# Kernel optimization log

Hardware: AMD Instinct MI355X
Metric: run time of the kernel (lower is better)

Reference implementation:

```python
import jax, jax.numpy as jnp
import numpy as np

S1 = 4096  # seq_len1
S2 = 4096  # seq_len2
D = 64     # in_dim1 == in_dim2
H = 2      # num_heads
KD = 1     # k_dim
VD = 1     # v_dim
EPS_NORM = 1e-12  # F.normalize eps
EPS_BN = 1e-5


def setup_inputs() -> dict:
    key = jax.random.key(0)
    ks = jax.random.split(key, 11)
    f = lambda k, s: jax.random.normal(k, s, dtype=jnp.float32)
    return {
        "x1": f(ks[0], (1, S1, D)),
        "x2": f(ks[1], (1, S2, D)),
        "Wq": f(ks[2], (D, H * KD)) * 0.1,   # proj_q1 (no bias)
        "Wk": f(ks[3], (D, H * KD)) * 0.1,   # proj_k2 (no bias)
        "Wv": f(ks[4], (D, H * VD)) * 0.1,   # proj_v2 (no bias)
        "Wo": f(ks[5], (H * VD, 2)) * 0.1,   # proj_o weight
        "bo": f(ks[6], (2,)) * 0.1,          # proj_o bias
        "Wg1": f(ks[7], (D, D)) * 0.1,       # CBN gamma MLP
        "Wg2": f(ks[8], (D, D)) * 0.1,
        "Wb1": f(ks[9], (D, D)) * 0.1,       # CBN beta MLP
        "Wb2": f(ks[10], (D, D)) * 0.1,
    }


def _l2norm_rows(x):
    # F.normalize(x, p=2, dim=1): divide by max(||row||, eps)
    n = jnp.sqrt(jnp.sum(x * x, axis=1, keepdims=True))
    return x / jnp.maximum(n, EPS_NORM)


def reference(x1, x2, Wq, Wk, Wv, Wo, bo, Wg1, Wg2, Wb1, Wb2):
    x1s, x2s = x1[0], x2[0]            # [S1,D], [S2,D] (batch squeezed, batch==1)
    # --- CBN stand-in: batchnorm of x2 conditioned on pooled x1 embedding ---
    h = x1s.mean(axis=0)               # [D]
    dg = jax.nn.relu(h @ Wg1) @ Wg2    # delta_gamma [D]
    db = jax.nn.relu(h @ Wb1) @ Wb2    # delta_beta  [D]
    mu = x2s.mean(axis=0)
    var = x2s.var(axis=0)
    v2_0 = (1.0 + dg) * (x2s - mu) * jax.lax.rsqrt(var + EPS_BN) + db  # [S2,D]
    # --- L2 normalizations ---
    v2n = _l2norm_rows(v2_0)[None]     # [1,S2,D]
    y1 = _l2norm_rows(x1s)[None]       # [1,S1,D]
    y2 = _l2norm_rows(x2s)[None]       # [1,S2,D]
    # --- tiny-head cross attention ---
    q = (y1 @ Wq).reshape(1, S1, H, KD)
    k = (y2 @ Wk).reshape(1, S2, H, KD)
    v = (v2n @ Wv).reshape(1, S2, H, VD)
    attn = jnp.einsum('bshk,bthk->bhst', q, k) / (KD ** 0.5)  # [1,H,S1,S2]
    attn = jax.nn.softmax(attn, axis=-1)
    out = jnp.einsum('bhst,bthd->bshd', attn, v).reshape(1, S1, H * VD)
    return jax.nn.sigmoid(out @ Wo + bo)  # [1,S1,2]
```

## Files before the change

### kernel.cpp

```cpp
#include <hip/hip_runtime.h>
#include <math.h>

#define NS1 4096
#define NS2 4096
#define ND  64

static constexpr int OFF_SUMX1 = 0;
static constexpr int OFF_SUMX2 = 64;
static constexpr int OFF_SSQX2 = 128;
static constexpr int OFF_SCALE = 192;
static constexpr int OFF_BETA  = 256;
static constexpr int OFF_MU    = 320;
static constexpr int OFF_KB    = 384;
static constexpr int OFF_Q     = 512;
static constexpr int OFF_KV    = 512 + 2 * 4096;
static constexpr int OFF_NUM   = OFF_KV + 4 * 4096;
static constexpr int OFF_DEN   = OFF_NUM + 2 * 4096;

__device__ inline float wred64(float v) {
    #pragma unroll
    for (int off = 32; off; off >>= 1) v += __shfl_xor(v, off);
    return v;
}

__global__ __launch_bounds__(256) void k_colred(const float* __restrict__ x1,
                                                const float* __restrict__ x2,
                                                float* __restrict__ ws) {
    int b = blockIdx.x;
    int tid = threadIdx.x;
    int w = tid >> 6, d = tid & 63;
    bool isx2 = (b >= 128);
    const float* x = isx2 ? x2 : x1;
    int row0 = (isx2 ? (b - 128) : b) * 32 + w * 8;
    float s = 0.f, ss = 0.f;
    #pragma unroll
    for (int i = 0; i < 8; ++i) {
        float v = x[(row0 + i) * ND + d];
        s += v; ss += v * v;
    }
    __shared__ float redS[256];
    __shared__ float redQ[256];
    redS[tid] = s; redQ[tid] = ss;
    __syncthreads();
    if (tid < 64) {
        float st = redS[tid] + redS[tid + 64] + redS[tid + 128] + redS[tid + 192];
        if (!isx2) {
            atomicAdd(&ws[OFF_SUMX1 + tid], st);
        } else {
            float sq = redQ[tid] + redQ[tid + 64] + redQ[tid + 128] + redQ[tid + 192];
            atomicAdd(&ws[OFF_SUMX2 + tid], st);
            atomicAdd(&ws[OFF_SSQX2 + tid], sq);
        }
    }
}

__global__ __launch_bounds__(64) void k_prep(const float* __restrict__ Wg1,
                                             const float* __restrict__ Wg2,
                                             const float* __restrict__ Wb1,
                                             const float* __restrict__ Wb2,
                                             const float* __restrict__ Wk,
                                             float* __restrict__ ws) {
    int d = threadIdx.x;
    __shared__ float h[64], ag[64], ab[64];
    h[d] = ws[OFF_SUMX1 + d] * (1.f / (float)NS1);
    __syncthreads();
    float tg = 0.f, tb = 0.f;
    #pragma unroll 8
    for (int j = 0; j < 64; ++j) {
        float hj = h[j];
        tg = fmaf(hj, Wg1[j * 64 + d], tg);
        tb = fmaf(hj, Wb1[j * 64 + d], tb);
    }
    ag[d] = fmaxf(tg, 0.f);
    ab[d] = fmaxf(tb, 0.f);
    __syncthreads();
    float dg = 0.f, db = 0.f;
    #pragma unroll 8
    for (int j = 0; j < 64; ++j) {
        dg = fmaf(ag[j], Wg2[j * 64 + d], dg);
        db = fmaf(ab[j], Wb2[j * 64 + d], db);
    }
    float mu = ws[OFF_SUMX2 + d] * (1.f / (float)NS2);
    float var = ws[OFF_SSQX2 + d] * (1.f / (float)NS2) - mu * mu;
    ws[OFF_SCALE + d] = (1.f + dg) * rsqrtf(var + 1e-5f);
    ws[OFF_BETA + d]  = db;
    ws[OFF_MU + d]    = mu;
    float k0 = Wk[d * 2 + 0], k1 = Wk[d * 2 + 1];
    float s0 = wred64(k0 * k0);
    float s1 = wred64(k1 * k1);
    if (d == 0) { ws[OFF_KB + 0] = sqrtf(s0); ws[OFF_KB + 1] = sqrtf(s1); }
}

__global__ __launch_bounds__(256) void k_proj(const float* __restrict__ x1,
                                              const float* __restrict__ x2,
                                              const float* __restrict__ Wq,
                                              const float* __restrict__ Wk,
                                              const float* __restrict__ Wv,
                                              float* __restrict__ ws) {
    int b = blockIdx.x;
    int w = threadIdx.x >> 6, d = threadIdx.x & 63;
    bool isx1 = (b >= 1024);
    int row = (isx1 ? (b - 1024) : b) * 4 + w;
    if (!isx1) {
        float x = x2[row * ND + d];
        float n2 = wred64(x * x);
        float y = x * (1.f / fmaxf(sqrtf(n2), 1e-12f));
        float vv = fmaf(ws[OFF_SCALE + d], x - ws[OFF_MU + d], ws[OFF_BETA + d]);
        float nv = wred64(vv * vv);
        float vn = vv * (1.f / fmaxf(sqrtf(nv), 1e-12f));
        float k0 = wred64(y  * Wk[d * 2 + 0]);
        float k1 = wred64(y  * Wk[d * 2 + 1]);
        float v0 = wred64(vn * Wv[d * 2 + 0]);
        float v1 = wred64(vn * Wv[d * 2 + 1]);
        if (d == 0) {
            ((float4*)(ws + OFF_KV))[row] = make_float4(k0, k1, v0, v1);
        }
    } else {
        float x = x1[row * ND + d];
        float n2 = wred64(x * x);
        float y = x * (1.f / fmaxf(sqrtf(n2), 1e-12f));
        float q0 = wred64(y * Wq[d * 2 + 0]);
        float q1 = wred64(y * Wq[d * 2 + 1]);
        if (d == 0) {
            ws[OFF_Q + row] = q0;
            ws[OFF_Q + NS1 + row] = q1;
        }
    }
}

__global__ __launch_bounds__(256) void k_attn(const float* __restrict__ wsc,
                                              float* __restrict__ ws) {
    __shared__ float4 kv[128];
    int b = blockIdx.x;
    int sc = b & 15, tc = b >> 4;
    int tid = threadIdx.x;
    const float4* kvg = (const float4*)(wsc + OFF_KV);
    if (tid < 128) kv[tid] = kvg[tc * 128 + tid];
    __syncthreads();
    int s = sc * 256 + tid;
    float q0 = wsc[OFF_Q + s];
    float q1 = wsc[OFF_Q + NS1 + s];
    float m0 = fabsf(q0) * wsc[OFF_KB + 0];
    float m1 = fabsf(q1) * wsc[OFF_KB + 1];
    float n0 = 0.f, d0 = 0.f, n1 = 0.f, d1 = 0.f;
    #pragma unroll 4
    for (int i = 0; i < 128; ++i) {
        float4 t = kv[i];
        float e0 = __expf(fmaf(q0, t.x, -m0));
        float e1 = __expf(fmaf(q1, t.y, -m1));
        n0 = fmaf(e0, t.z, n0); d0 += e0;
        n1 = fmaf(e1, t.w, n1); d1 += e1;
    }
    atomicAdd(&ws[OFF_NUM + s],        n0);
    atomicAdd(&ws[OFF_NUM + NS1 + s],  n1);
    atomicAdd(&ws[OFF_DEN + s],        d0);
    atomicAdd(&ws[OFF_DEN + NS1 + s],  d1);
}

__global__ __launch_bounds__(256) void k_out(const float* __restrict__ ws,
                                             const float* __restrict__ Wo,
                                             const float* __restrict__ bo,
                                             float* __restrict__ out) {
    int s = blockIdx.x * 256 + threadIdx.x;
    float o0 = ws[OFF_NUM + s]       / ws[OFF_DEN + s];
    float o1 = ws[OFF_NUM + NS1 + s] / ws[OFF_DEN + NS1 + s];
    float z0 = fmaf(o0, Wo[0], fmaf(o1, Wo[2], bo[0]));
    float z1 = fmaf(o0, Wo[1], fmaf(o1, Wo[3], bo[1]));
    out[s * 2 + 0] = 1.f / (1.f + __expf(-z0));
    out[s * 2 + 1] = 1.f / (1.f + __expf(-z1));
}

extern "C" void kernel_launch(void* const* d_in, const int* in_sizes, int n_in,
                              void* d_out, int out_size, void* d_ws, size_t ws_size,
                              hipStream_t stream) {
    const float* x1  = (const float*)d_in[0];
    const float* x2  = (const float*)d_in[1];
    const float* Wq  = (const float*)d_in[2];
    const float* Wk  = (const float*)d_in[3];
    const float* Wv  = (const float*)d_in[4];
    const float* Wo  = (const float*)d_in[5];
    const float* bo  = (const float*)d_in[6];
    const float* Wg1 = (const float*)d_in[7];
    const float* Wg2 = (const float*)d_in[8];
    const float* Wb1 = (const float*)d_in[9];
    const float* Wb2 = (const float*)d_in[10];
    float* ws  = (float*)d_ws;
    float* out = (float*)d_out;

    hipMemsetAsync((char*)d_ws + OFF_SUMX1 * 4, 0, 512 * 4, stream);
    hipMemsetAsync((char*)d_ws + OFF_NUM * 4,   0, 4 * NS1 * 4, stream);

    k_colred<<<256, 256, 0, stream>>>(x1, x2, ws);
    k_prep<<<1, 64, 0, stream>>>(Wg1, Wg2, Wb1, Wb2, Wk, ws);
    k_proj<<<2048, 256, 0, stream>>>(x1, x2, Wq, Wk, Wv, ws);
    k_attn<<<512, 256, 0, stream>>>(ws, ws);
    k_out<<<16, 256, 0, stream>>>(ws, Wo, bo, out);
}
```

Before: 100.2 us.

## Fuse prep into projection and attention into output, dropping atomics and a memset

Every projection block now recomputes the tiny CBN MLP redundantly instead of running a separate single-block prep kernel. Attention is restructured so each block owns 8 query rows over all 4096 keys, reducing in-block via shuffles and shared memory. This removes the global atomics, the NUM/DEN memset and the separate output kernel. It also switches to exp2f with pre-scaled log2e and cuts the launch count from five to three. The trade-off is redundant MLP work per block and higher register pressure from 8 rows of accumulators.

```diff
diff --git a/kernel.cpp b/kernel.cpp
--- a/kernel.cpp
+++ b/kernel.cpp
@@ -1,21 +1,14 @@
 #include <hip/hip_runtime.h>
 #include <math.h>
 
-#define NS1 4096
-#define NS2 4096
-#define ND  64
+#define NS 4096
+#define LOG2E 1.44269504088896f
 
 static constexpr int OFF_SUMX1 = 0;
 static constexpr int OFF_SUMX2 = 64;
 static constexpr int OFF_SSQX2 = 128;
-static constexpr int OFF_SCALE = 192;
-static constexpr int OFF_BETA  = 256;
-static constexpr int OFF_MU    = 320;
-static constexpr int OFF_KB    = 384;
-static constexpr int OFF_Q     = 512;
-static constexpr int OFF_KV    = 512 + 2 * 4096;
-static constexpr int OFF_NUM   = OFF_KV + 4 * 4096;
-static constexpr int OFF_DEN   = OFF_NUM + 2 * 4096;
+static constexpr int OFF_Q     = 256;
+static constexpr int OFF_KV    = 256 + 2*4096;
 
 __device__ inline float wred64(float v) {
     #pragma unroll
@@ -35,7 +28,7 @@
     float s = 0.f, ss = 0.f;
     #pragma unroll
     for (int i = 0; i < 8; ++i) {
-        float v = x[(row0 + i) * ND + d];
+        float v = x[(row0 + i) * 64 + d];
         s += v; ss += v * v;
     }
     __shared__ float redS[256];
@@ -54,120 +47,155 @@
     }
 }
 
-__global__ __launch_bounds__(64) void k_prep(const float* __restrict__ Wg1,
-                                             const float* __restrict__ Wg2,
-                                             const float* __restrict__ Wb1,
-                                             const float* __restrict__ Wb2,
-                                             const float* __restrict__ Wk,
-                                             float* __restrict__ ws) {
-    int d = threadIdx.x;
-    __shared__ float h[64], ag[64], ab[64];
-    h[d] = ws[OFF_SUMX1 + d] * (1.f / (float)NS1);
-    __syncthreads();
-    float tg = 0.f, tb = 0.f;
-    #pragma unroll 8
-    for (int j = 0; j < 64; ++j) {
-        float hj = h[j];
-        tg = fmaf(hj, Wg1[j * 64 + d], tg);
-        tb = fmaf(hj, Wb1[j * 64 + d], tb);
-    }
-    ag[d] = fmaxf(tg, 0.f);
-    ab[d] = fmaxf(tb, 0.f);
-    __syncthreads();
-    float dg = 0.f, db = 0.f;
-    #pragma unroll 8
-    for (int j = 0; j < 64; ++j) {
-        dg = fmaf(ag[j], Wg2[j * 64 + d], dg);
-        db = fmaf(ab[j], Wb2[j * 64 + d], db);
-    }
-    float mu = ws[OFF_SUMX2 + d] * (1.f / (float)NS2);
-    float var = ws[OFF_SSQX2 + d] * (1.f / (float)NS2) - mu * mu;
-    ws[OFF_SCALE + d] = (1.f + dg) * rsqrtf(var + 1e-5f);
-    ws[OFF_BETA + d]  = db;
-    ws[OFF_MU + d]    = mu;
-    float k0 = Wk[d * 2 + 0], k1 = Wk[d * 2 + 1];
-    float s0 = wred64(k0 * k0);
-    float s1 = wred64(k1 * k1);
-    if (d == 0) { ws[OFF_KB + 0] = sqrtf(s0); ws[OFF_KB + 1] = sqrtf(s1); }
-}
-
-__global__ __launch_bounds__(256) void k_proj(const float* __restrict__ x1,
-                                              const float* __restrict__ x2,
-                                              const float* __restrict__ Wq,
-                                              const float* __restrict__ Wk,
-                                              const float* __restrict__ Wv,
-                                              float* __restrict__ ws) {
-    int b = blockIdx.x;
-    int w = threadIdx.x >> 6, d = threadIdx.x & 63;
-    bool isx1 = (b >= 1024);
-    int row = (isx1 ? (b - 1024) : b) * 4 + w;
-    if (!isx1) {
-        float x = x2[row * ND + d];
-        float n2 = wred64(x * x);
-        float y = x * (1.f / fmaxf(sqrtf(n2), 1e-12f));
-        float vv = fmaf(ws[OFF_SCALE + d], x - ws[OFF_MU + d], ws[OFF_BETA + d]);
-        float nv = wred64(vv * vv);
-        float vn = vv * (1.f / fmaxf(sqrtf(nv), 1e-12f));
-        float k0 = wred64(y  * Wk[d * 2 + 0]);
-        float k1 = wred64(y  * Wk[d * 2 + 1]);
-        float v0 = wred64(vn * Wv[d * 2 + 0]);
-        float v1 = wred64(vn * Wv[d * 2 + 1]);
-        if (d == 0) {
-            ((float4*)(ws + OFF_KV))[row] = make_float4(k0, k1, v0, v1);
+__global__ __launch_bounds__(256) void k_prep_proj(const float* __restrict__ x1,
+                                                   const float* __restrict__ x2,
+                                                   const float* __restrict__ Wq,
+                                                   const float* __restrict__ Wk,
+                                                   const float* __restrict__ Wv,
+                                                   const float* __restrict__ Wg1,
+                                                   const float* __restrict__ Wg2,
+                                                   const float* __restrict__ Wb1,
+                                                   const float* __restrict__ Wb2,
+                                                   float* __restrict__ ws) {
+    int b = blockIdx.x, tid = threadIdx.x;
+    int w = tid >> 6, d = tid & 63;
+    if (b < 256) {
+        __shared__ float hsh[64], pg_[4][64], pb_[4][64], ag[64], ab[64];
+        __shared__ float scl[64], bta[64], mu[64];
+        if (tid < 64) hsh[tid] = ws[OFF_SUMX1 + tid] * (1.f / 4096.f);
+        __syncthreads();
+        float pg = 0.f, pb = 0.f;
+        #pragma unroll
+        for (int jj = 0; jj < 16; ++jj) {
+            int j = w * 16 + jj; float hj = hsh[j];
+            pg = fmaf(hj, Wg1[j * 64 + d], pg);
+            pb = fmaf(hj, Wb1[j * 64 + d], pb);
+        }
+        pg_[w][d] = pg; pb_[w][d] = pb;
+        __syncthreads();
+        if (w == 0) {
+            ag[d] = fmaxf(pg_[0][d] + pg_[1][d] + pg_[2][d] + pg_[3][d], 0.f);
+            ab[d] = fmaxf(pb_[0][d] + pb_[1][d] + pb_[2][d] + pb_[3][d], 0.f);
+        }
+        __syncthreads();
+        pg = 0.f; pb = 0.f;
+        #pragma unroll
+        for (int jj = 0; jj < 16; ++jj) {
+            int j = w * 16 + jj;
+            pg = fmaf(ag[j], Wg2[j * 64 + d], pg);
+            pb = fmaf(ab[j], Wb2[j * 64 + d], pb);
+        }
+        pg_[w][d] = pg; pb_[w][d] = pb;
+        __syncthreads();
+        if (w == 0) {
+            float dg = pg_[0][d] + pg_[1][d] + pg_[2][d] + pg_[3][d];
+            float db = pb_[0][d] + pb_[1][d] + pb_[2][d] + pb_[3][d];
+            float muv = ws[OFF_SUMX2 + d] * (1.f / 4096.f);
+            float var = ws[OFF_SSQX2 + d] * (1.f / 4096.f) - muv * muv;
+            scl[d] = (1.f + dg) * rsqrtf(var + 1e-5f);
+            bta[d] = db; mu[d] = muv;
+        }
+        __syncthreads();
+        float wk0 = Wk[d * 2 + 0], wk1 = Wk[d * 2 + 1];
+        float wv0 = Wv[d * 2 + 0], wv1 = Wv[d * 2 + 1];
+        float4* kvo = (float4*)(ws + OFF_KV);
+        #pragma unroll
+        for (int r = 0; r < 4; ++r) {
+            int row = b * 16 + w * 4 + r;
+            float x = x2[row * 64 + d];
+            float n2 = wred64(x * x);
+            float y = x * (1.f / fmaxf(sqrtf(n2), 1e-12f));
+            float vv = fmaf(scl[d], x - mu[d], bta[d]);
+            float nv = wred64(vv * vv);
+            float vn = vv * (1.f / fmaxf(sqrtf(nv), 1e-12f));
+            float k0 = wred64(y * wk0),  k1 = wred64(y * wk1);
+            float v0 = wred64(vn * wv0), v1 = wred64(vn * wv1);
+            if (d == 0) kvo[row] = make_float4(k0, k1, v0, v1);
         }
     } else {
-        float x = x1[row * ND + d];
-        float n2 = wred64(x * x);
-        float y = x * (1.f / fmaxf(sqrtf(n2), 1e-12f));
-        float q0 = wred64(y * Wq[d * 2 + 0]);
-        float q1 = wred64(y * Wq[d * 2 + 1]);
-        if (d == 0) {
-            ws[OFF_Q + row] = q0;
-            ws[OFF_Q + NS1 + row] = q1;
-        }
-    }
-}
-
-__global__ __launch_bounds__(256) void k_attn(const float* __restrict__ wsc,
-                                              float* __restrict__ ws) {
-    __shared__ float4 kv[128];
-    int b = blockIdx.x;
-    int sc = b & 15, tc = b >> 4;
-    int tid = threadIdx.x;
-    const float4* kvg = (const float4*)(wsc + OFF_KV);
-    if (tid < 128) kv[tid] = kvg[tc * 128 + tid];
-    __syncthreads();
-    int s = sc * 256 + tid;
-    float q0 = wsc[OFF_Q + s];
-    float q1 = wsc[OFF_Q + NS1 + s];
-    float m0 = fabsf(q0) * wsc[OFF_KB + 0];
-    float m1 = fabsf(q1) * wsc[OFF_KB + 1];
-    float n0 = 0.f, d0 = 0.f, n1 = 0.f, d1 = 0.f;
-    #pragma unroll 4
-    for (int i = 0; i < 128; ++i) {
-        float4 t = kv[i];
-        float e0 = __expf(fmaf(q0, t.x, -m0));
-        float e1 = __expf(fmaf(q1, t.y, -m1));
-        n0 = fmaf(e0, t.z, n0); d0 += e0;
-        n1 = fmaf(e1, t.w, n1); d1 += e1;
-    }
-    atomicAdd(&ws[OFF_NUM + s],        n0);
-    atomicAdd(&ws[OFF_NUM + NS1 + s],  n1);
-    atomicAdd(&ws[OFF_DEN + s],        d0);
-    atomicAdd(&ws[OFF_DEN + NS1 + s],  d1);
-}
-
-__global__ __launch_bounds__(256) void k_out(const float* __restrict__ ws,
-                                             const float* __restrict__ Wo,
-                                             const float* __restrict__ bo,
-                                             float* __restrict__ out) {
-    int s = blockIdx.x * 256 + threadIdx.x;
-    float o0 = ws[OFF_NUM + s]       / ws[OFF_DEN + s];
-    float o1 = ws[OFF_NUM + NS1 + s] / ws[OFF_DEN + NS1 + s];
-    float z0 = fmaf(o0, Wo[0], fmaf(o1, Wo[2], bo[0]));
-    float z1 = fmaf(o0, Wo[1], fmaf(o1, Wo[3], bo[1]));
-    out[s * 2 + 0] = 1.f / (1.f + __expf(-z0));
-    out[s * 2 + 1] = 1.f / (1.f + __expf(-z1));
+        float wq0 = Wq[d * 2 + 0], wq1 = Wq[d * 2 + 1];
+        #pragma unroll
+        for (int r = 0; r < 4; ++r) {
+            int row = (b - 256) * 16 + w * 4 + r;
+            float x = x1[row * 64 + d];
+            float n2 = wred64(x * x);
+            float y = x * (1.f / fmaxf(sqrtf(n2), 1e-12f));
+            float q0 = wred64(y * wq0), q1 = wred64(y * wq1);
+            if (d == 0) { ws[OFF_Q + row] = q0; ws[OFF_Q + 4096 + row] = q1; }
+        }
+    }
+}
+
+__global__ __launch_bounds__(256) void k_attn_out(const float* __restrict__ ws,
+                                                  const float* __restrict__ Wk,
+                                                  const float* __restrict__ Wo,
+                                                  const float* __restrict__ bo,
+                                                  float* __restrict__ out) {
+    int b = blockIdx.x, tid = threadIdx.x;
+    int w = tid >> 6, lane = tid & 63;
+    __shared__ float kb[2];
+    __shared__ float qsh[2][8];
+    if (w == 0) {
+        float c0 = Wk[lane * 2 + 0], c1 = Wk[lane * 2 + 1];
+        float s0 = wred64(c0 * c0), s1 = wred64(c1 * c1);
+        if (lane == 0) { kb[0] = sqrtf(s0); kb[1] = sqrtf(s1); }
+    }
+    if (tid >= 64 && tid < 72) {
+        int si = tid - 64;
+        qsh[0][si] = ws[OFF_Q + b * 8 + si];
+        qsh[1][si] = ws[OFF_Q + 4096 + b * 8 + si];
+    }
+    __syncthreads();
+    float q0r[8], q1r[8], m0r[8], m1r[8];
+    #pragma unroll
+    for (int si = 0; si < 8; ++si) {
+        q0r[si] = qsh[0][si] * LOG2E;
+        q1r[si] = qsh[1][si] * LOG2E;
+        m0r[si] = fabsf(q0r[si]) * kb[0];
+        m1r[si] = fabsf(q1r[si]) * kb[1];
+    }
+    float n0[8], d0[8], n1[8], d1[8];
+    #pragma unroll
+    for (int si = 0; si < 8; ++si) { n0[si] = 0.f; d0[si] = 0.f; n1[si] = 0.f; d1[si] = 0.f; }
+    const float4* kvg = (const float4*)(ws + OFF_KV);
+    for (int i = 0; i < 16; ++i) {
+        float4 t = kvg[i * 256 + tid];
+        #pragma unroll
+        for (int si = 0; si < 8; ++si) {
+            float e0 = exp2f(fmaf(q0r[si], t.x, -m0r[si]));
+            n0[si] = fmaf(e0, t.z, n0[si]); d0[si] += e0;
+            float e1 = exp2f(fmaf(q1r[si], t.y, -m1r[si]));
+            n1[si] = fmaf(e1, t.w, n1[si]); d1[si] += e1;
+        }
+    }
+    #pragma unroll
+    for (int si = 0; si < 8; ++si) {
+        n0[si] = wred64(n0[si]); d0[si] = wred64(d0[si]);
+        n1[si] = wred64(n1[si]); d1[si] = wred64(d1[si]);
+    }
+    __shared__ float red[4][32];
+    if (lane == 0) {
+        #pragma unroll
+        for (int si = 0; si < 8; ++si) {
+            red[w][si]      = n0[si];
+            red[w][8 + si]  = d0[si];
+            red[w][16 + si] = n1[si];
+            red[w][24 + si] = d1[si];
+        }
+    }
+    __syncthreads();
+    __shared__ float fin[32];
+    if (tid < 32) fin[tid] = red[0][tid] + red[1][tid] + red[2][tid] + red[3][tid];
+    __syncthreads();
+    if (tid < 8) {
+        float o0 = fin[tid]      / fin[8 + tid];
+        float o1 = fin[16 + tid] / fin[24 + tid];
+        float z0 = fmaf(o0, Wo[0], fmaf(o1, Wo[2], bo[0]));
+        float z1 = fmaf(o0, Wo[1], fmaf(o1, Wo[3], bo[1]));
+        int s = b * 8 + tid;
+        out[s * 2 + 0] = 1.f / (1.f + __expf(-z0));
+        out[s * 2 + 1] = 1.f / (1.f + __expf(-z1));
+    }
 }
 
 extern "C" void kernel_launch(void* const* d_in, const int* in_sizes, int n_in,
@@ -187,12 +215,9 @@
     float* ws  = (float*)d_ws;
     float* out = (float*)d_out;
 
-    hipMemsetAsync((char*)d_ws + OFF_SUMX1 * 4, 0, 512 * 4, stream);
-    hipMemsetAsync((char*)d_ws + OFF_NUM * 4,   0, 4 * NS1 * 4, stream);
+    hipMemsetAsync(d_ws, 0, 192 * 4, stream);
 
     k_colred<<<256, 256, 0, stream>>>(x1, x2, ws);
-    k_prep<<<1, 64, 0, stream>>>(Wg1, Wg2, Wb1, Wb2, Wk, ws);
-    k_proj<<<2048, 256, 0, stream>>>(x1, x2, Wq, Wk, Wv, ws);
-    k_attn<<<512, 256, 0, stream>>>(ws, ws);
-    k_out<<<16, 256, 0, stream>>>(ws, Wo, bo, out);
-}
+    k_prep_proj<<<512, 256, 0, stream>>>(x1, x2, Wq, Wk, Wv, Wg1, Wg2, Wb1, Wb2, ws);
+    k_attn_out<<<512, 256, 0, stream>>>(ws, Wk, Wo, bo, out);
+}
```

Result: no change. 100.0 us, median of 2 (-0.2%).
